# Performance work log

Measured on AMD Instinct MI355X. Metric: run time of the kernel, lower is better.

The kernel has to match this reference:

```python
import jax, jax.numpy as jnp
import numpy as np

B, IMSIZE, D, L, M, H = 8, 128, 64, 1, 16384, 100
N = B * IMSIZE * IMSIZE


def _build_edges(size, length):
    # build_perception: each pixel connects to all pixels within Chebyshev radius `length`
    ii, jj = np.meshgrid(np.arange(size), np.arange(size), indexing='ij')
    src, dst = [], []
    for dx in range(-length, length + 1):
        for dy in range(-length, length + 1):
            ok = (ii + dx >= 0) & (ii + dx < size) & (jj + dy >= 0) & (jj + dy < size)
            src.append((ii * size + jj)[ok])
            dst.append(((ii + dx) * size + (jj + dy))[ok])
    return np.concatenate(src), np.concatenate(dst)


def setup_inputs() -> dict:
    key = jax.random.key(0)
    ks = jax.random.split(key, 12)
    x = jax.random.normal(ks[0], (N, D), jnp.float32)  # RDN pixel features, flattened
    cluster = jax.random.randint(ks[1], (N,), 0, M).astype(jnp.int32)  # affinity-pool assignment
    s, d = _build_edges(IMSIZE, L)
    offs = (np.arange(B) * IMSIZE * IMSIZE)[:, None]
    edge_src = jnp.asarray((s[None] + offs).reshape(-1), jnp.int32)
    edge_dst = jnp.asarray((d[None] + offs).reshape(-1), jnp.int32)
    ii, jj = np.meshgrid(np.arange(IMSIZE), np.arange(IMSIZE), indexing='ij')
    g = np.stack([ii, jj], -1).reshape(-1, 2).astype(np.float32) / IMSIZE
    coords = jnp.asarray(np.tile(g, (B, 1)))  # spatial_coords.repeat(batch, 1)
    init = lambda k, sh: jax.random.normal(k, sh, jnp.float32) * 0.05
    params = dict(
        W1=init(ks[2], (D + 4, H)), b1=jnp.zeros((H,), jnp.float32),
        W2=init(ks[3], (H, H)), b2=jnp.zeros((H,), jnp.float32),
        W3=init(ks[4], (H, D)), b3=jnp.zeros((D,), jnp.float32),
        Wr=init(ks[5], (D, D)), Wn=init(ks[6], (D, D)), bg=jnp.zeros((D,), jnp.float32),
        Q1w=init(ks[7], (D, H)), Q1b=jnp.zeros((H,), jnp.float32),
        Q2w=init(ks[8], (H, H)), Q2b=jnp.zeros((H,), jnp.float32),
        Q3w=init(ks[9], (H, H)), Q3b=jnp.zeros((H,), jnp.float32),
        Q4w=init(ks[10], (H, 18)), Q4b=jnp.zeros((18,), jnp.float32),
    )
    out = dict(x=x, coords=coords, cluster=cluster, edge_src=edge_src, edge_dst=edge_dst)
    out.update(params)
    return out


def _render_qtr(G, feats):
    # RenderQTR, vectorized over the 3 channels: quadratic texture rendering per pixel
    centers, paras = feats[:, :2], feats[:, 2:20].reshape(-1, 3, 6)
    dx = (G[:, 0] - centers[:, 0])[:, None]
    dy = (G[:, 1] - centers[:, 1])[:, None]
    a, ah, aw, ahh, aww, ahw = (paras[:, :, k] for k in range(6))
    return a + ah * dx + aw * dy + ahh * dx * dx + aww * dy * dy + ahw * dx * dy


def reference(x, coords, cluster, edge_src, edge_dst, W1, b1, W2, b2, W3, b3, Wr, Wn, bg, Q1w, Q1b, Q2w, Q2b, Q3w, Q3b, Q4w, Q4b):
    # --- affinity-aggregation pooling (scatter-mean coarsening) ---
    cnt = jnp.maximum(jax.ops.segment_sum(jnp.ones((N, 1), x.dtype), cluster, num_segments=M), 1.0)
    xp = jax.ops.segment_sum(x, cluster, num_segments=M) / cnt
    cent = jax.ops.segment_sum(coords, cluster, num_segments=M) / cnt          # scatter_mean centroids
    mom = jax.ops.segment_sum(coords * coords, cluster, num_segments=M) / cnt  # scatter_mean moments
    # --- node transform FCBlock on [feat, 10*centroid, 10*moment] ---
    h = jnp.concatenate([xp, 10.0 * cent, 10.0 * mom], axis=-1)
    h = jax.nn.relu(h @ W1 + b1)
    h = jax.nn.relu(h @ W2 + b2)
    h = h @ W3 + b3
    # --- GraphConv(aggr='max') on cluster-coarsened edges (index-chase) ---
    cs, cd = cluster[edge_src], cluster[edge_dst]
    agg = jax.ops.segment_max((h @ Wn)[cs], cd, num_segments=M)
    agg = jnp.where(jnp.isfinite(agg), agg, 0.0)  # empty segments -> 0
    feat = h @ Wr + agg + bg
    # --- node_to_qtr_p2 FCBlock -> joint spatial features ---
    q = jax.nn.relu(feat @ Q1w + Q1b)
    q = jax.nn.relu(q @ Q2w + Q2b)
    q = jax.nn.relu(q @ Q3w + Q3b)
    q = q @ Q4w + Q4b
    jsf = jnp.concatenate([q, cent], axis=-1)[cluster]  # un-pool gather back to pixel nodes
    recon = _render_qtr(coords, jsf)                     # [N, 3]
    return recon.reshape(B, IMSIZE * IMSIZE, 3)          # to_dense_batch (equal-size batches)
```

## Files before the change

kernel.cpp:

```cpp
#include <hip/hip_runtime.h>
#include <hip/hip_fp16.h>
#include <cmath>

#define SSZ    128
#define SS     (SSZ*SSZ)
#define NB     8
#define NNODES (NB*SS)
#define DD     64
#define MM     16384
#define HH     100
#define BINCAP 64
#define KP     136
#define WSLOT  (112*KP)

typedef _Float16 f16x8 __attribute__((ext_vector_type(8)));
typedef _Float16 f16x2 __attribute__((ext_vector_type(2)));
typedef float    f32x4 __attribute__((ext_vector_type(4)));

__device__ __forceinline__ f16x2 hmax2(f16x2 a, f16x2 b) {
    f16x2 r;
    r.x = (a.x > b.x) ? a.x : b.x;
    r.y = (a.y > b.y) ? a.y : b.y;
    return r;
}

__device__ __forceinline__ f16x8 hmax8(f16x8 a, f16x8 b) {
    f16x8 r;
    #pragma unroll
    for (int i = 0; i < 8; i++) r[i] = (a[i] > b[i]) ? a[i] : b[i];
    return r;
}

__device__ __forceinline__ f16x8 shfl_xor16B(f16x8 v, int mask) {
    union { f16x8 h; int i[4]; } u;
    u.h = v;
    #pragma unroll
    for (int t = 0; t < 4; t++) u.i[t] = __shfl_xor(u.i[t], mask);
    return u.h;
}

__global__ void k_prep(const float* __restrict__ W1, const float* __restrict__ W2,
                       const float* __restrict__ W3, const float* __restrict__ Wn,
                       const float* __restrict__ Wr, const float* __restrict__ Q1w,
                       const float* __restrict__ Q2w, const float* __restrict__ Q3w,
                       const float* __restrict__ Q4w, __half* __restrict__ Wt,
                       int* __restrict__ binCnt) {
    int idx = blockIdx.x * 256 + threadIdx.x;
    if (idx < MM) binCnt[idx] = 0;
    if (idx >= 9 * WSLOT) return;
    int mat = idx / WSLOT, rem = idx - mat * WSLOT;
    int n = rem / KP, k = rem - n * KP;
    const float* src; int K, N;
    switch (mat) {
        case 0: src = W1;  K = 68;  N = 100; break;
        case 1: src = W2;  K = 100; N = 100; break;
        case 2: src = W3;  K = 100; N = 64;  break;
        case 3: src = Wn;  K = 64;  N = 64;  break;
        case 4: src = Wr;  K = 64;  N = 64;  break;
        case 5: src = Q1w; K = 64;  N = 100; break;
        case 6: src = Q2w; K = 100; N = 100; break;
        case 7: src = Q3w; K = 100; N = 100; break;
        default:src = Q4w; K = 100; N = 18;  break;
    }
    float v = (n < N && k < K) ? src[k * N + n] : 0.0f;
    Wt[idx] = __float2half(v);
}

__global__ void k_scatter(const int* __restrict__ cluster,
                          int* __restrict__ binCnt, int* __restrict__ nodeList,
                          int* __restrict__ posOf) {
    int n = blockIdx.x * 256 + threadIdx.x;
    if (n >= NNODES) return;
    int c = cluster[n];
    int pos = atomicAdd(&binCnt[c], 1);
    if (pos < BINCAP) {
        nodeList[c * BINCAP + pos] = n;
        posOf[n] = pos;
    } else {
        posOf[n] = BINCAP;
    }
}

template<int KC, int NT>
__device__ __forceinline__ void mfma_stage(
    const _Float16* __restrict__ inBuf, _Float16* __restrict__ outBuf,
    const _Float16* __restrict__ Wt, const float* __restrict__ bias,
    int Nout, bool relu, int w, int lane) {
    const int m = lane & 15, q = lane >> 4;
    f16x8 a[KC];
    #pragma unroll
    for (int kc = 0; kc < KC; kc++)
        a[kc] = *(const f16x8*)&inBuf[m * KP + kc * 32 + q * 8];
    #pragma unroll
    for (int tt = 0; tt < (NT + 3) / 4; tt++) {
        const int t = w + tt * 4;
        if (t >= NT) break;
        f32x4 acc = {0.0f, 0.0f, 0.0f, 0.0f};
        #pragma unroll
        for (int kc = 0; kc < KC; kc++) {
            f16x8 b = *(const f16x8*)&Wt[(16 * t + m) * KP + kc * 32 + q * 8];
            acc = __builtin_amdgcn_mfma_f32_16x16x32_f16(a[kc], b, acc, 0, 0, 0);
        }
        const int n = 16 * t + m;
        const float bb = (n < Nout) ? bias[n] : 0.0f;
        #pragma unroll
        for (int r = 0; r < 4; r++) {
            float c = acc[r] + bb;
            if (relu) c = fmaxf(c, 0.0f);
            if (n < Nout) outBuf[(q * 4 + r) * KP + n] = (_Float16)c;
        }
    }
}

__global__ __launch_bounds__(256) void k_mlp1(
    const float* __restrict__ x,
    const int* __restrict__ binCnt, const int* __restrict__ nodeList,
    const __half* __restrict__ WtAll,
    const float* __restrict__ b1, const float* __restrict__ b2,
    const float* __restrict__ b3, const float* __restrict__ bg,
    __half* __restrict__ hWnOut, float* __restrict__ featP,
    float* __restrict__ jsf) {
    __shared__ __align__(16) _Float16 sb0[16 * KP];
    __shared__ __align__(16) _Float16 sb1[16 * KP];
    const _Float16* Wt = (const _Float16*)WtAll;
    const int tid = threadIdx.x, lane = tid & 63, w = tid >> 6;
    const int c0 = blockIdx.x * 16;
    const int m = lane & 15, q = lane >> 4;

    int cnts[4], nls[4];
    #pragma unroll
    for (int cc = 0; cc < 4; cc++) {
        const int c = c0 + w * 4 + cc;
        int ct = binCnt[c];
        cnts[cc] = (ct > BINCAP) ? BINCAP : ct;
        nls[cc]  = nodeList[c * BINCAP + lane];
    }

    #pragma unroll
    for (int cc = 0; cc < 4; cc++) {
        const int cnt = cnts[cc];
        float gx = 0.0f, gy = 0.0f, g2 = 0.0f, g3 = 0.0f;
        if (lane < cnt) {
            int pos = nls[cc] & (SS - 1);
            gx = (float)(pos >> 7) * 0.0078125f;
            gy = (float)(pos & 127) * 0.0078125f;
            g2 = gx * gx; g3 = gy * gy;
        }
        #pragma unroll
        for (int d = 1; d < 64; d <<= 1) {
            gx += __shfl_xor(gx, d); gy += __shfl_xor(gy, d);
            g2 += __shfl_xor(g2, d); g3 += __shfl_xor(g3, d);
        }
        float t[16];
        #pragma unroll
        for (int u = 0; u < 16; u++) {
            int n = __shfl(nls[cc], u);
            int ns = (u < cnt) ? n : 0;
            t[u] = x[(size_t)ns * 64 + lane];
        }
        float s = 0.0f;
        #pragma unroll
        for (int u = 0; u < 16; u++) s += (u < cnt) ? t[u] : 0.0f;
        for (int i = 16; i < cnt; i++)
            s += x[(size_t)__shfl(nls[cc], i) * 64 + lane];

        const int ci = w * 4 + cc;
        const int c  = c0 + ci;
        float fcnt = fmaxf((float)cnt, 1.0f);
        sb0[ci * KP + lane] = (_Float16)(s / fcnt);
        if (lane == 0) {
            float cx = gx / fcnt, cy = gy / fcnt;
            sb0[ci * KP + 64] = (_Float16)(10.0f * cx);
            sb0[ci * KP + 65] = (_Float16)(10.0f * cy);
            sb0[ci * KP + 66] = (_Float16)(10.0f * g2 / fcnt);
            sb0[ci * KP + 67] = (_Float16)(10.0f * g3 / fcnt);
            jsf[c * 20 + 18] = cx;
            jsf[c * 20 + 19] = cy;
        }
    }
    for (int i = tid; i < 16 * 68; i += 256) {
        int r = i / 68, k = 68 + (i - r * 68);
        sb0[r * KP + k] = (_Float16)0.0f;
    }
    for (int i = tid; i < 16 * 36; i += 256) {
        int r = i / 36, k = 100 + (i - r * 36);
        sb1[r * KP + k] = (_Float16)0.0f;
    }
    __syncthreads();

    mfma_stage<3, 7>(sb0, sb1, Wt + 0 * WSLOT, b1, 100, true,  w, lane);
    __syncthreads();
    mfma_stage<4, 7>(sb1, sb0, Wt + 1 * WSLOT, b2, 100, true,  w, lane);
    __syncthreads();
    mfma_stage<4, 4>(sb0, sb1, Wt + 2 * WSLOT, b3, 64,  false, w, lane);
    __syncthreads();

    {
        const _Float16* Wnt = Wt + 3 * WSLOT;
        const _Float16* Wrt = Wt + 4 * WSLOT;
        f16x8 a0 = *(const f16x8*)&sb1[m * KP + q * 8];
        f16x8 a1 = *(const f16x8*)&sb1[m * KP + 32 + q * 8];
        const int t = w;
        f16x8 bn0 = *(const f16x8*)&Wnt[(16 * t + m) * KP + q * 8];
        f16x8 bn1 = *(const f16x8*)&Wnt[(16 * t + m) * KP + 32 + q * 8];
        f16x8 br0 = *(const f16x8*)&Wrt[(16 * t + m) * KP + q * 8];
        f16x8 br1 = *(const f16x8*)&Wrt[(16 * t + m) * KP + 32 + q * 8];
        f32x4 an = {0.0f, 0.0f, 0.0f, 0.0f};
        f32x4 ar = {0.0f, 0.0f, 0.0f, 0.0f};
        an = __builtin_amdgcn_mfma_f32_16x16x32_f16(a0, bn0, an, 0, 0, 0);
        an = __builtin_amdgcn_mfma_f32_16x16x32_f16(a1, bn1, an, 0, 0, 0);
        ar = __builtin_amdgcn_mfma_f32_16x16x32_f16(a0, br0, ar, 0, 0, 0);
        ar = __builtin_amdgcn_mfma_f32_16x16x32_f16(a1, br1, ar, 0, 0, 0);
        const int n = 16 * t + m;
        const float bgv = bg[n];
        #pragma unroll
        for (int r = 0; r < 4; r++) {
            int row = c0 + q * 4 + r;
            hWnOut[row * 64 + n] = __float2half(an[r]);
            featP [row * 64 + n] = ar[r] + bgv;
        }
    }
}

__global__ __launch_bounds__(512) void k_hvmax(
    const int* __restrict__ cluster, const int* __restrict__ posOf,
    const __half* __restrict__ hWn, __half* __restrict__ vmaxPerm) {
    __shared__ f16x2 hm[10][16][32];
    const int w = threadIdx.x >> 6, lane = threadIdx.x & 63;
    const int half = lane >> 5, lh = lane & 31;
    const int blk  = blockIdx.x;
    const int b    = blk >> 7;
    const int rem  = blk & 127;
    const int r0   = (rem >> 3) << 3;
    const int j0   = (rem & 7) << 4;
    const int base = b * SS;
    const f16x2 NEGH = {(_Float16)-65504.0f, (_Float16)-65504.0f};

    const int p0 = base + (r0 + w) * SSZ + j0;
    int c2 = 0, pos2 = BINCAP;
    if (lane < 16) {
        c2   = cluster[p0 + lane];
        pos2 = posOf[p0 + lane];
    }

    {
        const int s = (w << 1) | half;
        if (s < 10) {
            int gi = r0 - 1 + s;
            if (gi < 0 || gi >= SSZ) {
                #pragma unroll
                for (int k = 0; k < 16; k++) hm[s][k][lh] = NEGH;
            } else {
                int rowbase = base + gi * SSZ;
                int jl = j0 - 1 + lh;
                int cid = 0;
                if (lh < 18 && jl >= 0 && jl < SSZ) cid = cluster[rowbase + jl];
                f16x2 val[18];
                #pragma unroll
                for (int p = 0; p < 18; p++) {
                    int jp = j0 - 1 + p;
                    int cp = __shfl(cid, (half << 5) + p);
                    val[p] = NEGH;
                    if (jp >= 0 && jp < SSZ)
                        val[p] = *(const f16x2*)&hWn[(cp << 6) + (lh << 1)];
                }
                #pragma unroll
                for (int k = 0; k < 16; k++)
                    hm[s][k][lh] = hmax2(hmax2(val[k], val[k + 1]), val[k + 2]);
            }
        }
    }
    __syncthreads();

    {
        #pragma unroll
        for (int kk = 0; kk < 8; kk++) {
            const int k = (half << 3) + kk;
            f16x2 v = hmax2(hmax2(hm[w][k][lh], hm[w + 1][k][lh]),
                            hm[w + 2][k][lh]);
            int cK   = __shfl(c2, k);
            int posK = __shfl(pos2, k);
            if (posK < BINCAP)
                *(f16x2*)&vmaxPerm[((size_t)(cK * BINCAP + posK) << 6) + (lh << 1)] = v;
        }
    }
}

__global__ __launch_bounds__(256) void k_qmlp(
    const float* __restrict__ featP, const __half* __restrict__ vmaxPerm,
    const int* __restrict__ binCnt, const int* __restrict__ nodeList,
    const __half* __restrict__ WtAll,
    const float* __restrict__ Q1b, const float* __restrict__ Q2b,
    const float* __restrict__ Q3b, const float* __restrict__ Q4b,
    const float* __restrict__ jsf, float* __restrict__ out) {
    __shared__ __align__(16) _Float16 sb0[16 * KP];
    __shared__ __align__(16) _Float16 sb1[16 * KP];
    __shared__ float jsfT[16][20];
    const _Float16* Wt = (const _Float16*)WtAll;
    const int tid = threadIdx.x, lane = tid & 63, w = tid >> 6;
    const int c0 = blockIdx.x * 16;
    const int m = lane & 15, q = lane >> 4;

    int cnts[4];
    #pragma unroll
    for (int cc = 0; cc < 4; cc++) {
        int ct = binCnt[c0 + w * 4 + cc];
        cnts[cc] = (ct > BINCAP) ? BINCAP : ct;
    }
    {
        const f16x8 NEG8 = {(_Float16)-65504.0f, (_Float16)-65504.0f,
                            (_Float16)-65504.0f, (_Float16)-65504.0f,
                            (_Float16)-65504.0f, (_Float16)-65504.0f,
                            (_Float16)-65504.0f, (_Float16)-65504.0f};
        const int row = lane >> 3;
        f16x8 vb0[4], vb1[4];
        #pragma unroll
        for (int cc = 0; cc < 4; cc++) {
            const int c = c0 + w * 4 + cc;
            const _Float16* vp = (const _Float16*)vmaxPerm +
                                 ((size_t)c * BINCAP << 6);
            vb0[cc] = *(const f16x8*)&vp[lane * 8];
            const _Float16* vp1 = (cnts[cc] > 8) ? vp + 512 : vp;
            vb1[cc] = *(const f16x8*)&vp1[lane * 8];
        }
        #pragma unroll
        for (int cc = 0; cc < 4; cc++) {
            const int ci = w * 4 + cc, c = c0 + ci;
            const int cnt = cnts[cc];
            f16x8 a0 = (row < cnt)     ? vb0[cc] : NEG8;
            f16x8 a1 = (row + 8 < cnt) ? vb1[cc] : NEG8;
            f16x8 mx = hmax8(a0, a1);
            const _Float16* vp = (const _Float16*)vmaxPerm +
                                 ((size_t)c * BINCAP << 6);
            for (int bb = 2; (bb << 3) < cnt; bb++) {
                int r2 = (bb << 3) + row;
                f16x8 vv = *(const f16x8*)&vp[(bb << 9) + lane * 8];
                if (r2 < cnt) mx = hmax8(mx, vv);
            }
            mx = hmax8(mx, shfl_xor16B(mx, 8));
            mx = hmax8(mx, shfl_xor16B(mx, 16));
            mx = hmax8(mx, shfl_xor16B(mx, 32));
            if (lane < 8) {
                const float4* fp4 = (const float4*)&featP[(size_t)c * 64 + lane * 8];
                float4 f0 = fp4[0], f1 = fp4[1];
                f16x8 o;
                if (cnt == 0) {
                    o[0] = (_Float16)f0.x; o[1] = (_Float16)f0.y;
                    o[2] = (_Float16)f0.z; o[3] = (_Float16)f0.w;
                    o[4] = (_Float16)f1.x; o[5] = (_Float16)f1.y;
                    o[6] = (_Float16)f1.z; o[7] = (_Float16)f1.w;
                } else {
                    o[0] = (_Float16)(f0.x + (float)mx[0]);
                    o[1] = (_Float16)(f0.y + (float)mx[1]);
                    o[2] = (_Float16)(f0.z + (float)mx[2]);
                    o[3] = (_Float16)(f0.w + (float)mx[3]);
                    o[4] = (_Float16)(f1.x + (float)mx[4]);
                    o[5] = (_Float16)(f1.y + (float)mx[5]);
                    o[6] = (_Float16)(f1.z + (float)mx[6]);
                    o[7] = (_Float16)(f1.w + (float)mx[7]);
                }
                *(f16x8*)&sb0[ci * KP + lane * 8] = o;
            }
        }
    }
    for (int i = tid; i < 16 * 36; i += 256) {
        int r = i / 36, k = 100 + (i - r * 36);
        sb0[r * KP + k] = (_Float16)0.0f;
    }
    for (int i = tid; i < 16 * 36; i += 256) {
        int r = i / 36, k = 100 + (i - r * 36);
        sb1[r * KP + k] = (_Float16)0.0f;
    }
    if (tid < 32)
        jsfT[tid >> 1][18 + (tid & 1)] = jsf[(c0 + (tid >> 1)) * 20 + 18 + (tid & 1)];
    __syncthreads();

    mfma_stage<2, 7>(sb0, sb1, Wt + 5 * WSLOT, Q1b, 100, true, w, lane);
    __syncthreads();
    mfma_stage<4, 7>(sb1, sb0, Wt + 6 * WSLOT, Q2b, 100, true, w, lane);
    __syncthreads();
    mfma_stage<4, 7>(sb0, sb1, Wt + 7 * WSLOT, Q3b, 100, true, w, lane);
    __syncthreads();

    if (w < 2) {
        const _Float16* Q4t = Wt + 8 * WSLOT;
        f16x8 a[4];
        #pragma unroll
        for (int kc = 0; kc < 4; kc++)
            a[kc] = *(const f16x8*)&sb1[m * KP + kc * 32 + q * 8];
        const int t = w;
        f32x4 acc = {0.0f, 0.0f, 0.0f, 0.0f};
        #pragma unroll
        for (int kc = 0; kc < 4; kc++) {
            f16x8 b = *(const f16x8*)&Q4t[(16 * t + m) * KP + kc * 32 + q * 8];
            acc = __builtin_amdgcn_mfma_f32_16x16x32_f16(a[kc], b, acc, 0, 0, 0);
        }
        const int n = 16 * t + m;
        if (n < 18) {
            const float bb = Q4b[n];
            #pragma unroll
            for (int r = 0; r < 4; r++)
                jsfT[q * 4 + r][n] = acc[r] + bb;
        }
    }
    __syncthreads();

    {
        const int ci = tid >> 4;
        const int c  = c0 + ci;
        int cnt = binCnt[c];
        if (cnt > BINCAP) cnt = BINCAP;
        const float* fv = jsfT[ci];
        for (int slot = tid & 15; slot < cnt; slot += 16) {
            int n = nodeList[c * BINCAP + slot];
            int pos = n & (SS - 1);
            float gx = (float)(pos >> 7) * 0.0078125f;
            float gy = (float)(pos & 127) * 0.0078125f;
            float dx = gx - fv[0];
            float dy = gy - fv[1];
            #pragma unroll
            for (int r = 0; r < 3; r++) {
                float a   = fv[2 + r * 6 + 0];
                float ah  = fv[2 + r * 6 + 1];
                float aw  = fv[2 + r * 6 + 2];
                float ahh = fv[2 + r * 6 + 3];
                float aww = fv[2 + r * 6 + 4];
                float ahw = fv[2 + r * 6 + 5];
                out[n * 3 + r] = a + ah * dx + aw * dy + ahh * dx * dx
                               + aww * dy * dy + ahw * dx * dy;
            }
        }
    }
}

extern "C" void kernel_launch(void* const* d_in, const int* in_sizes, int n_in,
                              void* d_out, int out_size, void* d_ws, size_t ws_size,
                              hipStream_t stream) {
    const float* x       = (const float*)d_in[0];
    const int*   cluster = (const int*)  d_in[2];
    const float* W1  = (const float*)d_in[5];
    const float* b1  = (const float*)d_in[6];
    const float* W2  = (const float*)d_in[7];
    const float* b2  = (const float*)d_in[8];
    const float* W3  = (const float*)d_in[9];
    const float* b3  = (const float*)d_in[10];
    const float* Wr  = (const float*)d_in[11];
    const float* Wn  = (const float*)d_in[12];
    const float* bg  = (const float*)d_in[13];
    const float* Q1w = (const float*)d_in[14];
    const float* Q1b = (const float*)d_in[15];
    const float* Q2w = (const float*)d_in[16];
    const float* Q2b = (const float*)d_in[17];
    const float* Q3w = (const float*)d_in[18];
    const float* Q3b = (const float*)d_in[19];
    const float* Q4w = (const float*)d_in[20];
    const float* Q4b = (const float*)d_in[21];
    float* out = (float*)d_out;

    int*    binCnt   = (int*)d_ws;
    int*    nodeList = binCnt + MM;
    int*    posOf    = nodeList + MM * BINCAP;
    float*  featP    = (float*)(posOf + NNODES);
    float*  jsf      = featP + MM * 64;
    __half* hWnH     = (__half*)(jsf + MM * 20);
    __half* vmaxPerm = hWnH + MM * 64;
    __half* WtH      = vmaxPerm + (size_t)MM * BINCAP * 64;

    k_prep   <<<(9 * WSLOT + 255) / 256, 256, 0, stream>>>(W1, W2, W3, Wn, Wr,
                                                           Q1w, Q2w, Q3w, Q4w,
                                                           WtH, binCnt);
    k_scatter<<<(NNODES + 255) / 256, 256, 0, stream>>>(cluster, binCnt,
                                                        nodeList, posOf);
    k_mlp1   <<<MM / 16, 256, 0, stream>>>(x, binCnt, nodeList, WtH,
                                           b1, b2, b3, bg, hWnH, featP, jsf);
    k_hvmax  <<<1024, 512, 0, stream>>>(cluster, posOf, hWnH, vmaxPerm);
    k_qmlp   <<<MM / 16, 256, 0, stream>>>(featP, vmaxPerm, binCnt, nodeList,
                                           WtH, Q1b, Q2b, Q3b, Q4b, jsf, out);
}
```

Before: 163.4 us.

## Merge weight prep into scatter kernel and restructure gather loads in mlp1

Moves the weight transpose/convert work out of the bin-reset kernel and into extra blocks of the scatter kernel, so the weight-prep blocks run alongside the atomic binning. The weight write is re-indexed so consecutive threads read source weights contiguously. In k_mlp1 the per-cluster feature gathers are hoisted: the first 8 rows for all 4 clusters are issued up front, and the next 8 only when the count exceeds 8. This cuts wasted loads of node 0 and exposes more memory-level parallelism. The second vmax load is likewise skipped for small bins.

Result: no change. 161.4 us (-1.2%).

```diff
diff --git a/kernel.cpp b/kernel.cpp
--- a/kernel.cpp
+++ b/kernel.cpp
@@ -12,6 +12,8 @@
 #define BINCAP 64
 #define KP     136
 #define WSLOT  (112*KP)
+#define NODEBLK (NNODES/256)
+#define WPREPBLK ((9*WSLOT+255)/256)
 
 typedef _Float16 f16x8 __attribute__((ext_vector_type(8)));
 typedef _Float16 f16x2 __attribute__((ext_vector_type(2)));
@@ -39,17 +41,36 @@
     return u.h;
 }
 
-__global__ void k_prep(const float* __restrict__ W1, const float* __restrict__ W2,
-                       const float* __restrict__ W3, const float* __restrict__ Wn,
-                       const float* __restrict__ Wr, const float* __restrict__ Q1w,
-                       const float* __restrict__ Q2w, const float* __restrict__ Q3w,
-                       const float* __restrict__ Q4w, __half* __restrict__ Wt,
-                       int* __restrict__ binCnt) {
+__global__ void k_prep(int* __restrict__ binCnt) {
     int idx = blockIdx.x * 256 + threadIdx.x;
     if (idx < MM) binCnt[idx] = 0;
+}
+
+__global__ void k_scatter(const int* __restrict__ cluster,
+                          int* __restrict__ binCnt, int* __restrict__ nodeList,
+                          int* __restrict__ posOf,
+                          const float* __restrict__ W1, const float* __restrict__ W2,
+                          const float* __restrict__ W3, const float* __restrict__ Wn,
+                          const float* __restrict__ Wr, const float* __restrict__ Q1w,
+                          const float* __restrict__ Q2w, const float* __restrict__ Q3w,
+                          const float* __restrict__ Q4w, __half* __restrict__ Wt) {
+    const int b = blockIdx.x;
+    if (b < NODEBLK) {
+        int n = b * 256 + threadIdx.x;
+        int c = cluster[n];
+        int pos = atomicAdd(&binCnt[c], 1);
+        if (pos < BINCAP) {
+            nodeList[c * BINCAP + pos] = n;
+            posOf[n] = pos;
+        } else {
+            posOf[n] = BINCAP;
+        }
+        return;
+    }
+    int idx = (b - NODEBLK) * 256 + threadIdx.x;
     if (idx >= 9 * WSLOT) return;
     int mat = idx / WSLOT, rem = idx - mat * WSLOT;
-    int n = rem / KP, k = rem - n * KP;
+    int kk = rem / 112, nn = rem - kk * 112;
     const float* src; int K, N;
     switch (mat) {
         case 0: src = W1;  K = 68;  N = 100; break;
@@ -62,23 +83,8 @@
         case 7: src = Q3w; K = 100; N = 100; break;
         default:src = Q4w; K = 100; N = 18;  break;
     }
-    float v = (n < N && k < K) ? src[k * N + n] : 0.0f;
-    Wt[idx] = __float2half(v);
-}
-
-__global__ void k_scatter(const int* __restrict__ cluster,
-                          int* __restrict__ binCnt, int* __restrict__ nodeList,
-                          int* __restrict__ posOf) {
-    int n = blockIdx.x * 256 + threadIdx.x;
-    if (n >= NNODES) return;
-    int c = cluster[n];
-    int pos = atomicAdd(&binCnt[c], 1);
-    if (pos < BINCAP) {
-        nodeList[c * BINCAP + pos] = n;
-        posOf[n] = pos;
-    } else {
-        posOf[n] = BINCAP;
-    }
+    float v = (nn < N && kk < K) ? src[kk * N + nn] : 0.0f;
+    Wt[mat * WSLOT + nn * KP + kk] = __float2half(v);
 }
 
 template<int KC, int NT>
@@ -136,11 +142,21 @@
         nls[cc]  = nodeList[c * BINCAP + lane];
     }
 
+    float t0[4][8];
     #pragma unroll
     for (int cc = 0; cc < 4; cc++) {
-        const int cnt = cnts[cc];
+        #pragma unroll
+        for (int u = 0; u < 8; u++) {
+            int n = __shfl(nls[cc], u);
+            int ns = (u < cnts[cc]) ? n : 0;
+            t0[cc][u] = x[(size_t)ns * 64 + lane];
+        }
+    }
+    float bgx[4], bgy[4], bg2[4], bg3[4];
+    #pragma unroll
+    for (int cc = 0; cc < 4; cc++) {
         float gx = 0.0f, gy = 0.0f, g2 = 0.0f, g3 = 0.0f;
-        if (lane < cnt) {
+        if (lane < cnts[cc]) {
             int pos = nls[cc] & (SS - 1);
             gx = (float)(pos >> 7) * 0.0078125f;
             gy = (float)(pos & 127) * 0.0078125f;
@@ -151,29 +167,38 @@
             gx += __shfl_xor(gx, d); gy += __shfl_xor(gy, d);
             g2 += __shfl_xor(g2, d); g3 += __shfl_xor(g3, d);
         }
-        float t[16];
-        #pragma unroll
-        for (int u = 0; u < 16; u++) {
-            int n = __shfl(nls[cc], u);
-            int ns = (u < cnt) ? n : 0;
-            t[u] = x[(size_t)ns * 64 + lane];
-        }
+        bgx[cc] = gx; bgy[cc] = gy; bg2[cc] = g2; bg3[cc] = g3;
+    }
+    #pragma unroll
+    for (int cc = 0; cc < 4; cc++) {
+        const int cnt = cnts[cc];
         float s = 0.0f;
         #pragma unroll
-        for (int u = 0; u < 16; u++) s += (u < cnt) ? t[u] : 0.0f;
-        for (int i = 16; i < cnt; i++)
-            s += x[(size_t)__shfl(nls[cc], i) * 64 + lane];
-
+        for (int u = 0; u < 8; u++) s += (u < cnt) ? t0[cc][u] : 0.0f;
+        if (cnt > 8) {
+            float t1[8];
+            #pragma unroll
+            for (int u = 0; u < 8; u++) {
+                int i = 8 + u;
+                int n = __shfl(nls[cc], i);
+                int ns = (i < cnt) ? n : 0;
+                t1[u] = x[(size_t)ns * 64 + lane];
+            }
+            #pragma unroll
+            for (int u = 0; u < 8; u++) s += (8 + u < cnt) ? t1[u] : 0.0f;
+            for (int i = 16; i < cnt; i++)
+                s += x[(size_t)__shfl(nls[cc], i) * 64 + lane];
+        }
         const int ci = w * 4 + cc;
         const int c  = c0 + ci;
         float fcnt = fmaxf((float)cnt, 1.0f);
         sb0[ci * KP + lane] = (_Float16)(s / fcnt);
         if (lane == 0) {
-            float cx = gx / fcnt, cy = gy / fcnt;
+            float cx = bgx[cc] / fcnt, cy = bgy[cc] / fcnt;
             sb0[ci * KP + 64] = (_Float16)(10.0f * cx);
             sb0[ci * KP + 65] = (_Float16)(10.0f * cy);
-            sb0[ci * KP + 66] = (_Float16)(10.0f * g2 / fcnt);
-            sb0[ci * KP + 67] = (_Float16)(10.0f * g3 / fcnt);
+            sb0[ci * KP + 66] = (_Float16)(10.0f * bg2[cc] / fcnt);
+            sb0[ci * KP + 67] = (_Float16)(10.0f * bg3[cc] / fcnt);
             jsf[c * 20 + 18] = cx;
             jsf[c * 20 + 19] = cy;
         }
@@ -320,8 +345,10 @@
             const _Float16* vp = (const _Float16*)vmaxPerm +
                                  ((size_t)c * BINCAP << 6);
             vb0[cc] = *(const f16x8*)&vp[lane * 8];
-            const _Float16* vp1 = (cnts[cc] > 8) ? vp + 512 : vp;
-            vb1[cc] = *(const f16x8*)&vp1[lane * 8];
+            if (cnts[cc] > 8)
+                vb1[cc] = *(const f16x8*)&vp[512 + lane * 8];
+            else
+                vb1[cc] = NEG8;
         }
         #pragma unroll
         for (int cc = 0; cc < 4; cc++) {
@@ -466,11 +493,11 @@
     __half* vmaxPerm = hWnH + MM * 64;
     __half* WtH      = vmaxPerm + (size_t)MM * BINCAP * 64;
 
-    k_prep   <<<(9 * WSLOT + 255) / 256, 256, 0, stream>>>(W1, W2, W3, Wn, Wr,
-                                                           Q1w, Q2w, Q3w, Q4w,
-                                                           WtH, binCnt);
-    k_scatter<<<(NNODES + 255) / 256, 256, 0, stream>>>(cluster, binCnt,
-                                                        nodeList, posOf);
+    k_prep   <<<MM / 256, 256, 0, stream>>>(binCnt);
+    k_scatter<<<NODEBLK + WPREPBLK, 256, 0, stream>>>(cluster, binCnt,
+                                                      nodeList, posOf,
+                                                      W1, W2, W3, Wn, Wr,
+                                                      Q1w, Q2w, Q3w, Q4w, WtH);
     k_mlp1   <<<MM / 16, 256, 0, stream>>>(x, binCnt, nodeList, WtH,
                                            b1, b2, b3, bg, hWnH, featP, jsf);
     k_hvmax  <<<1024, 512, 0, stream>>>(cluster, posOf, hWnH, vmaxPerm);
```
